# Kernel optimization log

Hardware: AMD Instinct MI355X
Metric: run time of the kernel (lower is better)

Reference implementation:

```python
import jax, jax.numpy as jnp
import numpy as np

SHRINK_THRES = 0.0025
EPS_SHRINK = 1e-12
EPS_NORM = 1e-12


def setup_inputs() -> dict:
    key = jax.random.key(0)
    k1, k2 = jax.random.split(key)
    B, C, H, W = 32, 256, 32, 32
    mem_dim, fea_dim = 2000, 256
    x = jax.random.normal(k1, (B, C, H, W), dtype=jnp.float32)
    stdv = 1.0 / np.sqrt(fea_dim)
    memMatrix = jax.random.uniform(k2, (mem_dim, fea_dim), dtype=jnp.float32,
                                   minval=-stdv, maxval=stdv)
    return {"x": x, "memMatrix": memMatrix}


def _hard_shrink_relu(a, lambd, eps=EPS_SHRINK):
    # relu(a - lambd) * a / (|a - lambd| + eps)
    return jax.nn.relu(a - lambd) * a / (jnp.abs(a - lambd) + eps)


def reference(x, memMatrix):
    B, C, H, W = x.shape
    mem_dim = memMatrix.shape[0]
    # [B,C,H,W] -> [B,H,W,C] -> [N,C]
    q = jnp.transpose(x, (0, 2, 3, 1)).reshape(-1, C)
    # attention addressing: [N, mem_dim]
    att = q @ memMatrix.T
    att = jax.nn.softmax(att, axis=1)
    # hard shrinkage + L1 renormalize
    att = _hard_shrink_relu(att, SHRINK_THRES)
    denom = jnp.maximum(jnp.sum(jnp.abs(att), axis=1, keepdims=True), EPS_NORM)
    att = att / denom
    # memory read: [N, C]
    out = att @ memMatrix
    # reshape back: y [B,C,H,W], att [B,mem_dim,H,W]
    y = jnp.transpose(out.reshape(B, H, W, C), (0, 3, 1, 2))
    att_map = jnp.transpose(att.reshape(B, H, W, mem_dim), (0, 3, 1, 2))
    return y, att_map
```

## Files before the change

kernel.cpp:

```cpp
#include <hip/hip_runtime.h>

#define B_   32
#define C_   256
#define HW_  1024
#define N_   32768
#define M_   2000
#define MP_  2048
#define K_   256

typedef __attribute__((ext_vector_type(8))) _Float16 f16x8;
typedef __attribute__((ext_vector_type(4))) float f32x4;

#define KCAP 32
#define AP   266

__global__ void prep_memS_kernel(const float* __restrict__ mem,
                                 _Float16* __restrict__ mh,
                                 _Float16* __restrict__ ml) {
  int m = blockIdx.x;
  int p = threadIdx.x;
  int c = ((p & 15) << 4) | (p >> 4);
  float v = (m < M_) ? mem[m * K_ + c] * 64.0f : 0.0f;
  _Float16 h = (_Float16)v;
  mh[m * K_ + p] = h;
  ml[m * K_ + p] = (_Float16)(v - (float)h);
}

__global__ __launch_bounds__(512, 1) void fused_kernel(
    const float* __restrict__ x,
    const _Float16* __restrict__ mh, const _Float16* __restrict__ ml,
    const float* __restrict__ mem,
    float* __restrict__ y, float* __restrict__ att) {
  __shared__ float xs[256][33];
  __shared__ _Float16 Ahs[32][AP];
  __shared__ _Float16 Als[32][AP];
  __shared__ float S_part[8][32];
  __shared__ float Sthr[32];
  __shared__ float inv[32];
  __shared__ unsigned int kcnt[32];
  __shared__ unsigned int km[32][KCAP];
  __shared__ float kp[32][KCAP];

  const int tid   = threadIdx.x;
  const int lane  = tid & 63;
  const int wave  = tid >> 6;
  const int row16 = lane & 15;
  const int quad  = lane >> 4;
  const int n0  = blockIdx.x * 32;
  const int b   = n0 >> 10;
  const int hw0 = n0 & 1023;
  const int mw  = wave * 256;

  {
    const int c = tid >> 1;
    const int h16 = (tid & 1) * 16;
    const float* src = x + ((size_t)b * C_ + c) * HW_ + hw0 + h16;
#pragma unroll
    for (int i = 0; i < 4; ++i)
      *(f32x4*)(&xs[c][h16 + i * 4]) = *(const f32x4*)(src + i * 4);
  }
  if (tid < 32) kcnt[tid] = 0;
  __syncthreads();

  {
    const int nl = tid >> 4;
    const int g  = tid & 15;
    f16x8 hi0, hi1, lo0, lo1;
#pragma unroll
    for (int u = 0; u < 8; ++u) {
      float v = xs[u * 16 + g][nl];
      _Float16 h = (_Float16)v;
      hi0[u] = h; lo0[u] = (_Float16)(v - (float)h);
    }
#pragma unroll
    for (int u = 0; u < 8; ++u) {
      float v = xs[(u + 8) * 16 + g][nl];
      _Float16 h = (_Float16)v;
      hi1[u] = h; lo1[u] = (_Float16)(v - (float)h);
    }
    *(f16x8*)(&Ahs[nl][g * 16])     = hi0;
    *(f16x8*)(&Ahs[nl][g * 16 + 8]) = hi1;
    *(f16x8*)(&Als[nl][g * 16])     = lo0;
    *(f16x8*)(&Als[nl][g * 16 + 8]) = lo1;
  }
  __syncthreads();

  f32x4 acc[2][16];
#pragma unroll
  for (int i = 0; i < 2; ++i)
#pragma unroll
    for (int j = 0; j < 16; ++j) acc[i][j] = (f32x4){0.f, 0.f, 0.f, 0.f};

  const _Float16* mhp = mh + (size_t)(mw + row16) * K_ + quad * 8;
  const _Float16* mlp = ml + (size_t)(mw + row16) * K_ + quad * 8;

#pragma unroll 1
  for (int ks = 0; ks < 8; ++ks) {
    const int ko = ks * 32 + quad * 8;
    f16x8 ah0 = *(const f16x8*)(&Ahs[row16][ko]);
    f16x8 ah1 = *(const f16x8*)(&Ahs[16 + row16][ko]);
    f16x8 al0 = *(const f16x8*)(&Als[row16][ko]);
    f16x8 al1 = *(const f16x8*)(&Als[16 + row16][ko]);
#pragma unroll
    for (int jg = 0; jg < 2; ++jg) {
      f16x8 bh[8], bl[8];
#pragma unroll
      for (int u = 0; u < 8; ++u) {
        const int j = jg * 8 + u;
        bh[u] = *(const f16x8*)(mhp + (size_t)j * 16 * K_ + ks * 32);
        bl[u] = *(const f16x8*)(mlp + (size_t)j * 16 * K_ + ks * 32);
      }
#pragma unroll
      for (int u = 0; u < 8; ++u) {
        const int j = jg * 8 + u;
        acc[0][j] = __builtin_amdgcn_mfma_f32_16x16x32_f16(ah0, bh[u], acc[0][j], 0, 0, 0);
        acc[1][j] = __builtin_amdgcn_mfma_f32_16x16x32_f16(ah1, bh[u], acc[1][j], 0, 0, 0);
        acc[0][j] = __builtin_amdgcn_mfma_f32_16x16x32_f16(al0, bh[u], acc[0][j], 0, 0, 0);
        acc[1][j] = __builtin_amdgcn_mfma_f32_16x16x32_f16(al1, bh[u], acc[1][j], 0, 0, 0);
        acc[0][j] = __builtin_amdgcn_mfma_f32_16x16x32_f16(ah0, bl[u], acc[0][j], 0, 0, 0);
        acc[1][j] = __builtin_amdgcn_mfma_f32_16x16x32_f16(ah1, bl[u], acc[1][j], 0, 0, 0);
      }
    }
  }

  const int maskj = (mw + 256 > M_) ? (M_ - mw) / 16 : 16;
#pragma unroll
  for (int i = 0; i < 2; ++i)
#pragma unroll
    for (int j = 0; j < 16; ++j)
#pragma unroll
      for (int r = 0; r < 4; ++r)
        acc[i][j][r] = (j < maskj) ? __expf(acc[i][j][r] * 0.015625f) : 0.f;

  const int nlb = quad * 4;
#pragma unroll
  for (int i = 0; i < 2; ++i)
#pragma unroll
    for (int r = 0; r < 4; ++r) {
      float s = 0.f;
#pragma unroll
      for (int j = 0; j < 16; ++j) s += acc[i][j][r];
      s += __shfl_xor(s, 1, 16);
      s += __shfl_xor(s, 2, 16);
      s += __shfl_xor(s, 4, 16);
      s += __shfl_xor(s, 8, 16);
      if (row16 == 0) S_part[wave][i * 16 + nlb + r] = s;
    }
  __syncthreads();
  if (tid < 32) {
    float s = 0.f;
#pragma unroll
    for (int w = 0; w < 8; ++w) s += S_part[w][tid];
    Sthr[tid] = 0.0025f * s;
  }
  __syncthreads();

#pragma unroll
  for (int i = 0; i < 2; ++i)
#pragma unroll
    for (int r = 0; r < 4; ++r) {
      const int nl = i * 16 + nlb + r;
      const float thr = Sthr[nl];
      float s2 = 0.f;
#pragma unroll
      for (int j = 0; j < 16; ++j) {
        const float e = acc[i][j][r];
        if (e > thr) {
          s2 += e;
          unsigned int pos = atomicAdd(&kcnt[nl], 1u);
          if (pos < (unsigned)KCAP) {
            km[nl][pos] = (unsigned)(mw + j * 16 + row16);
            kp[nl][pos] = e;
          }
        }
      }
      s2 += __shfl_xor(s2, 1, 16);
      s2 += __shfl_xor(s2, 2, 16);
      s2 += __shfl_xor(s2, 4, 16);
      s2 += __shfl_xor(s2, 8, 16);
      if (row16 == 0) S_part[wave][nl] = s2;
    }
  __syncthreads();
  if (tid < 32) {
    float s2 = 0.f;
#pragma unroll
    for (int w = 0; w < 8; ++w) s2 += S_part[w][tid];
    inv[tid] = (s2 > 0.f) ? 1.0f / s2 : 0.f;
  }
  __syncthreads();

#pragma unroll
  for (int i = 0; i < 2; ++i)
#pragma unroll
    for (int r = 0; r < 4; ++r) {
      const int nl = i * 16 + nlb + r;
      const float thr = Sthr[nl];
      const float iv = inv[nl];
#pragma unroll
      for (int j = 0; j < 16; ++j) {
        const float e = acc[i][j][r];
        acc[i][j][r] = (e > thr) ? e * iv : 0.f;
      }
    }

  {
    float* attb = att + (size_t)b * M_ * HW_ + hw0;
#pragma unroll
    for (int j = 0; j < 16; ++j) {
      if (mw + j * 16 < M_) {
        float* ar = attb + (size_t)(mw + j * 16 + row16) * HW_ + nlb;
        *(f32x4*)(ar)      = acc[0][j];
        *(f32x4*)(ar + 16) = acc[1][j];
      }
    }
  }

  {
    const int hwL = tid & 31;
    const int cq  = tid >> 5;
    unsigned int kc = kcnt[hwL];
    if (kc > (unsigned)KCAP) kc = KCAP;
    const float iv = inv[hwL];
    float yv[16];
#pragma unroll
    for (int ci = 0; ci < 16; ++ci) yv[ci] = 0.f;
#pragma unroll 1
    for (unsigned int k = 0; k < kc; ++k) {
      const float p = kp[hwL][k];
      const float* mrow = mem + (size_t)km[hwL][k] * K_ + cq;
#pragma unroll
      for (int ci = 0; ci < 16; ++ci)
        yv[ci] += p * mrow[ci * 16];
    }
    float* yb = y + (size_t)b * C_ * HW_ + hw0 + hwL;
#pragma unroll
    for (int ci = 0; ci < 16; ++ci)
      yb[(size_t)(ci * 16 + cq) * HW_] = yv[ci] * iv;
  }
}

extern "C" void kernel_launch(void* const* d_in, const int* in_sizes, int n_in,
                              void* d_out, int out_size, void* d_ws, size_t ws_size,
                              hipStream_t stream) {
  const float* x   = (const float*)d_in[0];
  const float* mem = (const float*)d_in[1];
  float* y       = (float*)d_out;
  float* att_out = (float*)d_out + (size_t)B_ * C_ * HW_;

  char* ws = (char*)d_ws;
  _Float16* mh = (_Float16*)ws;
  _Float16* ml = (_Float16*)(ws + (size_t)1024 * 1024);

  prep_memS_kernel<<<dim3(MP_), dim3(K_), 0, stream>>>(mem, mh, ml);
  fused_kernel<<<dim3(N_ / 32), dim3(512), 0, stream>>>(
      x, mh, ml, mem, y, att_out);
}
```

Before: 614.6 us.

## Stage memory matrix through double-buffered swizzled LDS with direct global-to-LDS loads

The memory matrix is repacked into one interleaved hi/lo fp16 buffer, grouped per K-step and XOR-swizzled. The fused kernel now streams it into a double-buffered shared-memory tile with global_load_lds, so the next chunk loads while MFMAs run on the current one. Each wave now covers a 32-row slice of every 256-row chunk instead of a contiguous 256-row block. This replaces per-wave scattered global loads of the B operand with coalesced staging, at the cost of a block barrier for every chunk (64 per block) and a larger LDS footprint that reuses the x staging area.

```diff
diff --git a/kernel.cpp b/kernel.cpp
--- a/kernel.cpp
+++ b/kernel.cpp
@@ -12,31 +12,36 @@
 typedef __attribute__((ext_vector_type(4))) float f32x4;
 
 #define KCAP 32
-#define AP   266
+#define AP   264
+
+#define MFMA16(a, b, c) __builtin_amdgcn_mfma_f32_16x16x32_f16(a, b, c, 0, 0, 0)
 
 __global__ void prep_memS_kernel(const float* __restrict__ mem,
-                                 _Float16* __restrict__ mh,
-                                 _Float16* __restrict__ ml) {
+                                 _Float16* __restrict__ mhs) {
   int m = blockIdx.x;
   int p = threadIdx.x;
   int c = ((p & 15) << 4) | (p >> 4);
   float v = (m < M_) ? mem[m * K_ + c] * 64.0f : 0.0f;
   _Float16 h = (_Float16)v;
-  mh[m * K_ + p] = h;
-  ml[m * K_ + p] = (_Float16)(v - (float)h);
+  _Float16 l = (_Float16)(v - (float)h);
+  int ks = p >> 5, kk = p & 31;
+  int sh = (kk >> 3) ^ (m & 7);
+  int sl = ((kk >> 3) + 4) ^ (m & 7);
+  size_t base = ((size_t)ks * MP_ + m) * 64;
+  mhs[base + sh * 8 + (kk & 7)] = h;
+  mhs[base + sl * 8 + (kk & 7)] = l;
 }
 
 __global__ __launch_bounds__(512, 1) void fused_kernel(
-    const float* __restrict__ x,
-    const _Float16* __restrict__ mh, const _Float16* __restrict__ ml,
+    const float* __restrict__ x, const _Float16* __restrict__ mhs,
     const float* __restrict__ mem,
     float* __restrict__ y, float* __restrict__ att) {
-  __shared__ float xs[256][33];
+  __shared__ _Float16 Bs[2][256 * 64];
   __shared__ _Float16 Ahs[32][AP];
   __shared__ _Float16 Als[32][AP];
   __shared__ float S_part[8][32];
   __shared__ float Sthr[32];
-  __shared__ float inv[32];
+  __shared__ float inv_s[32];
   __shared__ unsigned int kcnt[32];
   __shared__ unsigned int km[32][KCAP];
   __shared__ float kp[32][KCAP];
@@ -46,10 +51,12 @@
   const int wave  = tid >> 6;
   const int row16 = lane & 15;
   const int quad  = lane >> 4;
+  const int r7    = row16 & 7;
   const int n0  = blockIdx.x * 32;
   const int b   = n0 >> 10;
   const int hw0 = n0 & 1023;
-  const int mw  = wave * 256;
+
+  float (*xs)[33] = (float (*)[33])&Bs[0][0];
 
   {
     const int c = tid >> 1;
@@ -85,66 +92,92 @@
   }
   __syncthreads();
 
-  f32x4 acc[2][16];
-#pragma unroll
-  for (int i = 0; i < 2; ++i)
-#pragma unroll
-    for (int j = 0; j < 16; ++j) acc[i][j] = (f32x4){0.f, 0.f, 0.f, 0.f};
-
-  const _Float16* mhp = mh + (size_t)(mw + row16) * K_ + quad * 8;
-  const _Float16* mlp = ml + (size_t)(mw + row16) * K_ + quad * 8;
+#define STAGE(bufidx, unit) do {                                              \
+    const _Float16* gs_ = mhs + (size_t)(unit) * 16384;                       \
+    _Float16* ld_ = &Bs[bufidx][0];                                           \
+    _Pragma("unroll")                                                         \
+    for (int i_ = 0; i_ < 4; ++i_) {                                          \
+      __builtin_amdgcn_global_load_lds(                                       \
+        (const __attribute__((address_space(1))) unsigned int*)(gs_ + (i_ * 512 + tid) * 8), \
+        (__attribute__((address_space(3))) unsigned int*)(ld_ + (i_ * 512 + tid) * 8),       \
+        16, 0, 0);                                                            \
+    }                                                                         \
+  } while (0)
+
+  STAGE(0, 0);
+  __syncthreads();
+
+  f32x4 acc[8][2][2];
+#pragma unroll
+  for (int ch = 0; ch < 8; ++ch)
+#pragma unroll
+    for (int nf = 0; nf < 2; ++nf)
+#pragma unroll
+      for (int mf = 0; mf < 2; ++mf) acc[ch][nf][mf] = (f32x4){0.f, 0.f, 0.f, 0.f};
+
+  const int mA = wave * 32;
+  const int sH = (quad ^ r7) * 8;
+  const int sL = ((4 | quad) ^ r7) * 8;
 
 #pragma unroll 1
   for (int ks = 0; ks < 8; ++ks) {
-    const int ko = ks * 32 + quad * 8;
-    f16x8 ah0 = *(const f16x8*)(&Ahs[row16][ko]);
-    f16x8 ah1 = *(const f16x8*)(&Ahs[16 + row16][ko]);
-    f16x8 al0 = *(const f16x8*)(&Als[row16][ko]);
-    f16x8 al1 = *(const f16x8*)(&Als[16 + row16][ko]);
-#pragma unroll
-    for (int jg = 0; jg < 2; ++jg) {
-      f16x8 bh[8], bl[8];
-#pragma unroll
-      for (int u = 0; u < 8; ++u) {
-        const int j = jg * 8 + u;
-        bh[u] = *(const f16x8*)(mhp + (size_t)j * 16 * K_ + ks * 32);
-        bl[u] = *(const f16x8*)(mlp + (size_t)j * 16 * K_ + ks * 32);
-      }
-#pragma unroll
-      for (int u = 0; u < 8; ++u) {
-        const int j = jg * 8 + u;
-        acc[0][j] = __builtin_amdgcn_mfma_f32_16x16x32_f16(ah0, bh[u], acc[0][j], 0, 0, 0);
-        acc[1][j] = __builtin_amdgcn_mfma_f32_16x16x32_f16(ah1, bh[u], acc[1][j], 0, 0, 0);
-        acc[0][j] = __builtin_amdgcn_mfma_f32_16x16x32_f16(al0, bh[u], acc[0][j], 0, 0, 0);
-        acc[1][j] = __builtin_amdgcn_mfma_f32_16x16x32_f16(al1, bh[u], acc[1][j], 0, 0, 0);
-        acc[0][j] = __builtin_amdgcn_mfma_f32_16x16x32_f16(ah0, bl[u], acc[0][j], 0, 0, 0);
-        acc[1][j] = __builtin_amdgcn_mfma_f32_16x16x32_f16(ah1, bl[u], acc[1][j], 0, 0, 0);
-      }
-    }
-  }
-
-  const int maskj = (mw + 256 > M_) ? (M_ - mw) / 16 : 16;
-#pragma unroll
-  for (int i = 0; i < 2; ++i)
-#pragma unroll
-    for (int j = 0; j < 16; ++j)
-#pragma unroll
-      for (int r = 0; r < 4; ++r)
-        acc[i][j][r] = (j < maskj) ? __expf(acc[i][j][r] * 0.015625f) : 0.f;
+    f16x8 ah[2], al[2];
+#pragma unroll
+    for (int nf = 0; nf < 2; ++nf) {
+      ah[nf] = *(const f16x8*)(&Ahs[nf * 16 + row16][ks * 32 + quad * 8]);
+      al[nf] = *(const f16x8*)(&Als[nf * 16 + row16][ks * 32 + quad * 8]);
+    }
+#pragma unroll
+    for (int ch = 0; ch < 8; ++ch) {
+      if (ch < 7) { STAGE((ch + 1) & 1, ks * 8 + ch + 1); }
+      else if (ks < 7) { STAGE((ch + 1) & 1, ks * 8 + ch + 1); }
+      const _Float16* bp0 = &Bs[ch & 1][(mA + row16) * 64];
+      f16x8 bh0 = *(const f16x8*)(bp0 + sH);
+      f16x8 bl0 = *(const f16x8*)(bp0 + sL);
+      f16x8 bh1 = *(const f16x8*)(bp0 + 16 * 64 + sH);
+      f16x8 bl1 = *(const f16x8*)(bp0 + 16 * 64 + sL);
+      acc[ch][0][0] = MFMA16(ah[0], bh0, acc[ch][0][0]);
+      acc[ch][1][0] = MFMA16(ah[1], bh0, acc[ch][1][0]);
+      acc[ch][0][1] = MFMA16(ah[0], bh1, acc[ch][0][1]);
+      acc[ch][1][1] = MFMA16(ah[1], bh1, acc[ch][1][1]);
+      acc[ch][0][0] = MFMA16(al[0], bh0, acc[ch][0][0]);
+      acc[ch][1][0] = MFMA16(al[1], bh0, acc[ch][1][0]);
+      acc[ch][0][1] = MFMA16(al[0], bh1, acc[ch][0][1]);
+      acc[ch][1][1] = MFMA16(al[1], bh1, acc[ch][1][1]);
+      acc[ch][0][0] = MFMA16(ah[0], bl0, acc[ch][0][0]);
+      acc[ch][1][0] = MFMA16(ah[1], bl0, acc[ch][1][0]);
+      acc[ch][0][1] = MFMA16(ah[0], bl1, acc[ch][0][1]);
+      acc[ch][1][1] = MFMA16(ah[1], bl1, acc[ch][1][1]);
+      __syncthreads();
+    }
+  }
+
+#pragma unroll
+  for (int ch = 0; ch < 8; ++ch)
+#pragma unroll
+    for (int mf = 0; mf < 2; ++mf) {
+      const bool valid = (ch * 256 + mA + mf * 16) < M_;
+#pragma unroll
+      for (int nf = 0; nf < 2; ++nf)
+#pragma unroll
+        for (int r = 0; r < 4; ++r)
+          acc[ch][nf][mf][r] = valid ? __expf(acc[ch][nf][mf][r] * 0.015625f) : 0.f;
+    }
 
   const int nlb = quad * 4;
 #pragma unroll
-  for (int i = 0; i < 2; ++i)
+  for (int nf = 0; nf < 2; ++nf)
 #pragma unroll
     for (int r = 0; r < 4; ++r) {
       float s = 0.f;
 #pragma unroll
-      for (int j = 0; j < 16; ++j) s += acc[i][j][r];
+      for (int ch = 0; ch < 8; ++ch)
+        s += acc[ch][nf][0][r] + acc[ch][nf][1][r];
       s += __shfl_xor(s, 1, 16);
       s += __shfl_xor(s, 2, 16);
       s += __shfl_xor(s, 4, 16);
       s += __shfl_xor(s, 8, 16);
-      if (row16 == 0) S_part[wave][i * 16 + nlb + r] = s;
+      if (row16 == 0) S_part[wave][nf * 16 + nlb + r] = s;
     }
   __syncthreads();
   if (tid < 32) {
@@ -156,24 +189,26 @@
   __syncthreads();
 
 #pragma unroll
-  for (int i = 0; i < 2; ++i)
+  for (int nf = 0; nf < 2; ++nf)
 #pragma unroll
     for (int r = 0; r < 4; ++r) {
-      const int nl = i * 16 + nlb + r;
+      const int nl = nf * 16 + nlb + r;
       const float thr = Sthr[nl];
       float s2 = 0.f;
 #pragma unroll
-      for (int j = 0; j < 16; ++j) {
-        const float e = acc[i][j][r];
-        if (e > thr) {
-          s2 += e;
-          unsigned int pos = atomicAdd(&kcnt[nl], 1u);
-          if (pos < (unsigned)KCAP) {
-            km[nl][pos] = (unsigned)(mw + j * 16 + row16);
-            kp[nl][pos] = e;
+      for (int ch = 0; ch < 8; ++ch)
+#pragma unroll
+        for (int mf = 0; mf < 2; ++mf) {
+          const float e = acc[ch][nf][mf][r];
+          if (e > thr) {
+            s2 += e;
+            unsigned int pos = atomicAdd(&kcnt[nl], 1u);
+            if (pos < (unsigned)KCAP) {
+              km[nl][pos] = (unsigned)(ch * 256 + mA + mf * 16 + row16);
+              kp[nl][pos] = e;
+            }
           }
         }
-      }
       s2 += __shfl_xor(s2, 1, 16);
       s2 += __shfl_xor(s2, 2, 16);
       s2 += __shfl_xor(s2, 4, 16);
@@ -185,34 +220,39 @@
     float s2 = 0.f;
 #pragma unroll
     for (int w = 0; w < 8; ++w) s2 += S_part[w][tid];
-    inv[tid] = (s2 > 0.f) ? 1.0f / s2 : 0.f;
-  }
-  __syncthreads();
-
-#pragma unroll
-  for (int i = 0; i < 2; ++i)
-#pragma unroll
-    for (int r = 0; r < 4; ++r) {
-      const int nl = i * 16 + nlb + r;
-      const float thr = Sthr[nl];
-      const float iv = inv[nl];
-#pragma unroll
-      for (int j = 0; j < 16; ++j) {
-        const float e = acc[i][j][r];
-        acc[i][j][r] = (e > thr) ? e * iv : 0.f;
+    inv_s[tid] = (s2 > 0.f) ? 1.0f / s2 : 0.f;
+  }
+  __syncthreads();
+
+  {
+    f32x4 thr4[2], iv4[2];
+#pragma unroll
+    for (int nf = 0; nf < 2; ++nf)
+#pragma unroll
+      for (int r = 0; r < 4; ++r) {
+        thr4[nf][r] = Sthr[nf * 16 + nlb + r];
+        iv4[nf][r]  = inv_s[nf * 16 + nlb + r];
       }
-    }
-
-  {
     float* attb = att + (size_t)b * M_ * HW_ + hw0;
 #pragma unroll
-    for (int j = 0; j < 16; ++j) {
-      if (mw + j * 16 < M_) {
-        float* ar = attb + (size_t)(mw + j * 16 + row16) * HW_ + nlb;
-        *(f32x4*)(ar)      = acc[0][j];
-        *(f32x4*)(ar + 16) = acc[1][j];
+    for (int ch = 0; ch < 8; ++ch)
+#pragma unroll
+      for (int mf = 0; mf < 2; ++mf) {
+        if (ch * 256 + mA + mf * 16 < M_) {
+          const int m = ch * 256 + mA + mf * 16 + row16;
+          float* ar = attb + (size_t)m * HW_ + nlb;
+          f32x4 p0, p1;
+#pragma unroll
+          for (int r = 0; r < 4; ++r) {
+            const float e0 = acc[ch][0][mf][r];
+            const float e1 = acc[ch][1][mf][r];
+            p0[r] = (e0 > thr4[0][r]) ? e0 * iv4[0][r] : 0.f;
+            p1[r] = (e1 > thr4[1][r]) ? e1 * iv4[1][r] : 0.f;
+          }
+          *(f32x4*)(ar)      = p0;
+          *(f32x4*)(ar + 16) = p1;
+        }
       }
-    }
   }
 
   {
@@ -220,7 +260,7 @@
     const int cq  = tid >> 5;
     unsigned int kc = kcnt[hwL];
     if (kc > (unsigned)KCAP) kc = KCAP;
-    const float iv = inv[hwL];
+    const float iv = inv_s[hwL];
     float yv[16];
 #pragma unroll
     for (int ci = 0; ci < 16; ++ci) yv[ci] = 0.f;
@@ -237,6 +277,7 @@
     for (int ci = 0; ci < 16; ++ci)
       yb[(size_t)(ci * 16 + cq) * HW_] = yv[ci] * iv;
   }
+#undef STAGE
 }
 
 extern "C" void kernel_launch(void* const* d_in, const int* in_sizes, int n_in,
@@ -247,11 +288,9 @@
   float* y       = (float*)d_out;
   float* att_out = (float*)d_out + (size_t)B_ * C_ * HW_;
 
-  char* ws = (char*)d_ws;
-  _Float16* mh = (_Float16*)ws;
-  _Float16* ml = (_Float16*)(ws + (size_t)1024 * 1024);
-
-  prep_memS_kernel<<<dim3(MP_), dim3(K_), 0, stream>>>(mem, mh, ml);
+  _Float16* mhs = (_Float16*)d_ws;
+
+  prep_memS_kernel<<<dim3(MP_), dim3(K_), 0, stream>>>(mem, mhs);
   fused_kernel<<<dim3(N_ / 32), dim3(512), 0, stream>>>(
-      x, mh, ml, mem, y, att_out);
+      x, mhs, mem, y, att_out);
 }
```

Result: faster. 533.7 us (-13.2%).
